# Performance work log

Hardware: AMD Instinct MI355X
Metric: run time of the kernel (lower is better)

## Reference

```python
import jax, jax.numpy as jnp
import numpy as np

N_NODES = 100000
N_EDGES = 1600000
IN_FEATS, N_HIDDEN, N_CLASSES = 128, 128, 32


def setup_inputs() -> dict:
    key = jax.random.key(0)
    ks = jax.random.split(key, 9)
    x = jax.random.normal(ks[0], (N_NODES, IN_FEATS), dtype=jnp.float32)
    src = jax.random.randint(ks[1], (N_EDGES,), 0, N_NODES, dtype=jnp.int64)
    dst = jax.random.randint(ks[2], (N_EDGES,), 0, N_NODES, dtype=jnp.int64)
    s1 = 1.0 / np.sqrt(IN_FEATS)
    s2 = 1.0 / np.sqrt(N_HIDDEN)
    W1 = jax.random.uniform(ks[3], (IN_FEATS, N_HIDDEN), jnp.float32, -s1, s1)
    b1 = jnp.zeros((N_HIDDEN,), jnp.float32)
    W2 = jax.random.uniform(ks[4], (N_HIDDEN, N_HIDDEN), jnp.float32, -s2, s2)
    b2 = jnp.zeros((N_HIDDEN,), jnp.float32)
    W3 = jax.random.uniform(ks[5], (N_HIDDEN, N_CLASSES), jnp.float32, -s2, s2)
    b3 = jnp.zeros((N_CLASSES,), jnp.float32)
    return {"x": x, "W1": W1, "b1": b1, "W2": W2, "b2": b2, "W3": W3, "b3": b3,
            "src": src, "dst": dst}


def _norms(src, dst):
    ones = jnp.ones((src.shape[0],), jnp.float32)
    deg_out = jax.ops.segment_sum(ones, src, num_segments=N_NODES)
    deg_in = jax.ops.segment_sum(ones, dst, num_segments=N_NODES)
    inv_sqrt = lambda d: jnp.where(d > 0, jax.lax.rsqrt(jnp.maximum(d, 1.0)), 0.0)
    return inv_sqrt(deg_out), inv_sqrt(deg_in)


def _sgconv(h, W, b, src, dst, norm_src, norm_dst):
    # D^-1/2 A D^-1/2 h, then linear
    m = h * norm_src[:, None]          # scale by source (out-degree) norm
    msg = m[src]                        # [E, F] gather
    agg = jax.ops.segment_sum(msg, dst, num_segments=N_NODES)  # scatter-add
    agg = agg * norm_dst[:, None]
    return agg @ W + b


def reference(x, W1, b1, W2, b2, W3, b3, src, dst):
    norm_src, norm_dst = _norms(src, dst)
    h = _sgconv(x, W1, b1, src, dst, norm_src, norm_dst)
    h = jax.nn.relu(h)
    h = _sgconv(h, W2, b2, src, dst, norm_src, norm_dst)
    h = jax.nn.relu(h)
    h = _sgconv(h, W3, b3, src, dst, norm_src, norm_dst)
    return h
```

## Files before the change

kernel.cpp:

```cpp
#include <hip/hip_runtime.h>


constexpr int FEAT   = 128;
constexpr int STRIDE = 48;

typedef float f32x4 __attribute__((ext_vector_type(4)));
typedef short bf16x8 __attribute__((ext_vector_type(8)));

__device__ __forceinline__ unsigned short f2bf(float f) {
    unsigned int u = __builtin_bit_cast(unsigned int, f);
    unsigned int r = (u + 0x7FFFu + ((u >> 16) & 1u)) >> 16;
    return (unsigned short)r;
}
__device__ __forceinline__ float bflo(unsigned int u) {
    return __builtin_bit_cast(float, u << 16);
}
__device__ __forceinline__ float bfhi(unsigned int u) {
    return __builtin_bit_cast(float, u & 0xffff0000u);
}
__device__ __forceinline__ unsigned int pack2(float a, float b) {
    return (unsigned int)f2bf(a) | ((unsigned int)f2bf(b) << 16);
}

__global__ __launch_bounds__(256) void wfrag_kernel(const float* __restrict__ W1,
                                                    const float* __restrict__ W3,
                                                    unsigned short* __restrict__ f1,
                                                    unsigned short* __restrict__ f3)
{
    int idx = blockIdx.x * 256 + threadIdx.x;
    const float* W;
    unsigned short* f;
    int NC, i;
    if (idx < 2048)      { W = W1; f = f1; NC = 128; i = idx; }
    else if (idx < 2560) { W = W3; f = f3; NC = 32;  i = idx - 2048; }
    else return;
    int l  = i & 63;
    int k0 = (i >> 6) & 3;
    int n0 = i >> 8;
    int kb = k0 * 32 + (l >> 4) * 8;
    int n  = n0 * 16 + (l & 15);
    const float* wp = W + (size_t)kb * NC + n;
    uint4 v;
    v.x = pack2(wp[0],      wp[NC]);
    v.y = pack2(wp[2 * NC], wp[3 * NC]);
    v.z = pack2(wp[4 * NC], wp[5 * NC]);
    v.w = pack2(wp[6 * NC], wp[7 * NC]);
    *reinterpret_cast<uint4*>(&f[i * 8]) = v;
}

__global__ __launch_bounds__(256) void degree_fill_xw1_kernel(
    const int* __restrict__ src, const int* __restrict__ dst,
    const float* __restrict__ x, const unsigned short* __restrict__ w1frag,
    int* __restrict__ deg_out, int* __restrict__ deg_in,
    int* __restrict__ csr_pad, unsigned short* __restrict__ xw1,
    int N, int E)
{
    const int tid = threadIdx.x;
    const int g = (int)blockIdx.x / 5;
    const int m = (int)blockIdx.x % 5;

    if (m != 4) {
        int e = (g * 4 + m) * 256 + tid;
        if (e < E) {
            int s = src[e];
            int d = dst[e];
            atomicAdd(&deg_out[s], 1);
            int pos = atomicAdd(&deg_in[d], 1);
            if (pos < STRIDE)
                csr_pad[(size_t)d * STRIDE + pos] = s;
        }
        return;
    }

    const int wave = tid >> 6, lane = tid & 63;
    const int rowbase = g * 64 + wave * 16;
    const int arow = min(rowbase + (lane & 15), N - 1);
    const int koff = (lane >> 4) * 8;

    bf16x8 a[4];
    #pragma unroll
    for (int k0 = 0; k0 < 4; ++k0) {
        const float* xp = x + (size_t)arow * 128 + k0 * 32 + koff;
        float4 f0 = *reinterpret_cast<const float4*>(xp);
        float4 f1 = *reinterpret_cast<const float4*>(xp + 4);
        union { unsigned int u[4]; bf16x8 v; } r;
        r.u[0] = pack2(f0.x, f0.y); r.u[1] = pack2(f0.z, f0.w);
        r.u[2] = pack2(f1.x, f1.y); r.u[3] = pack2(f1.z, f1.w);
        a[k0] = r.v;
    }

    f32x4 acc[8];
    #pragma unroll
    for (int n0 = 0; n0 < 8; ++n0) acc[n0] = (f32x4)0.f;
    #pragma unroll
    for (int k0 = 0; k0 < 4; ++k0) {
        #pragma unroll
        for (int n0 = 0; n0 < 8; ++n0) {
            bf16x8 b = *reinterpret_cast<const bf16x8*>(&w1frag[((n0 * 4 + k0) * 64 + lane) * 8]);
            acc[n0] = __builtin_amdgcn_mfma_f32_16x16x32_bf16(a[k0], b, acc[n0], 0, 0, 0);
        }
    }

    const int colbase = lane & 15;
    const int rowoff = (lane >> 4) * 4;
    #pragma unroll
    for (int r = 0; r < 4; ++r) {
        const int grow = rowbase + rowoff + r;
        if (grow < N) {
            unsigned short* op = xw1 + (size_t)grow * 128 + colbase;
            #pragma unroll
            for (int n0 = 0; n0 < 8; ++n0)
                op[n0 * 16] = f2bf(acc[n0][r]);
        }
    }
}

__global__ __launch_bounds__(256) void norm_kernel(const int* __restrict__ dout,
                                                   const int* __restrict__ din,
                                                   float* __restrict__ nsrc,
                                                   float* __restrict__ ndst, int N)
{
    int i = blockIdx.x * 256 + threadIdx.x;
    if (i < N) {
        int a = dout[i], b = din[i];
        nsrc[i] = (a > 0) ? rsqrtf((float)a) : 0.f;
        ndst[i] = (b > 0) ? rsqrtf((float)b) : 0.f;
    }
}

__global__ __launch_bounds__(256) void gather1_kernel(const unsigned short* __restrict__ xw1,
                                                      const float* __restrict__ nsrc,
                                                      const float* __restrict__ ndst,
                                                      const int* __restrict__ deg_in,
                                                      const int* __restrict__ csr_pad,
                                                      const float* __restrict__ b1,
                                                      unsigned short* __restrict__ hb1,
                                                      int N)
{
    const int node = blockIdx.x * 16 + (threadIdx.x >> 4);
    const int c = (threadIdx.x & 15) * 8;
    if (node >= N) return;
    const int* idx = csr_pad + (size_t)node * STRIDE;
    const int deg = min(deg_in[node], STRIDE);
    float4 a0 = make_float4(0.f, 0.f, 0.f, 0.f);
    float4 a1 = make_float4(0.f, 0.f, 0.f, 0.f);
    int j = 0;
    for (; j + 8 <= deg; j += 8) {
        int s[8];
        float ns[8];
        #pragma unroll
        for (int u = 0; u < 8; ++u) s[u] = idx[j + u];
        #pragma unroll
        for (int u = 0; u < 8; ++u) ns[u] = nsrc[s[u]];
        #pragma unroll
        for (int u = 0; u < 8; ++u) {
            uint4 v = *reinterpret_cast<const uint4*>(xw1 + (size_t)s[u] * 128 + c);
            a0.x = fmaf(bflo(v.x), ns[u], a0.x);
            a0.y = fmaf(bfhi(v.x), ns[u], a0.y);
            a0.z = fmaf(bflo(v.y), ns[u], a0.z);
            a0.w = fmaf(bfhi(v.y), ns[u], a0.w);
            a1.x = fmaf(bflo(v.z), ns[u], a1.x);
            a1.y = fmaf(bfhi(v.z), ns[u], a1.y);
            a1.z = fmaf(bflo(v.w), ns[u], a1.z);
            a1.w = fmaf(bfhi(v.w), ns[u], a1.w);
        }
    }
    for (; j < deg; ++j) {
        int s0 = idx[j];
        float n0 = nsrc[s0];
        uint4 v = *reinterpret_cast<const uint4*>(xw1 + (size_t)s0 * 128 + c);
        a0.x = fmaf(bflo(v.x), n0, a0.x);
        a0.y = fmaf(bfhi(v.x), n0, a0.y);
        a0.z = fmaf(bflo(v.y), n0, a0.z);
        a0.w = fmaf(bfhi(v.y), n0, a0.w);
        a1.x = fmaf(bflo(v.z), n0, a1.x);
        a1.y = fmaf(bfhi(v.z), n0, a1.y);
        a1.z = fmaf(bflo(v.w), n0, a1.z);
        a1.w = fmaf(bfhi(v.w), n0, a1.w);
    }
    const float nd = ndst[node];
    const float nsn = nsrc[node];
    const float* bp = b1 + c;
    float v0 = fmaxf(a0.x * nd + bp[0], 0.f) * nsn;
    float v1 = fmaxf(a0.y * nd + bp[1], 0.f) * nsn;
    float v2 = fmaxf(a0.z * nd + bp[2], 0.f) * nsn;
    float v3 = fmaxf(a0.w * nd + bp[3], 0.f) * nsn;
    float v4 = fmaxf(a1.x * nd + bp[4], 0.f) * nsn;
    float v5 = fmaxf(a1.y * nd + bp[5], 0.f) * nsn;
    float v6 = fmaxf(a1.z * nd + bp[6], 0.f) * nsn;
    float v7 = fmaxf(a1.w * nd + bp[7], 0.f) * nsn;
    uint4 o;
    o.x = pack2(v0, v1); o.y = pack2(v2, v3);
    o.z = pack2(v4, v5); o.w = pack2(v6, v7);
    *reinterpret_cast<uint4*>(hb1 + (size_t)node * 128 + c) = o;
}

__global__ __launch_bounds__(256) void gather128_kernel(const unsigned short* __restrict__ hb,
                                                        const float* __restrict__ ndst,
                                                        const int* __restrict__ deg_in,
                                                        const int* __restrict__ csr_pad,
                                                        unsigned short* __restrict__ aggb,
                                                        int N)
{
    const int node = blockIdx.x * 16 + (threadIdx.x >> 4);
    const int c = (threadIdx.x & 15) * 8;
    if (node >= N) return;
    const int* idx = csr_pad + (size_t)node * STRIDE;
    const int deg = min(deg_in[node], STRIDE);
    float4 a0 = make_float4(0.f, 0.f, 0.f, 0.f);
    float4 a1 = make_float4(0.f, 0.f, 0.f, 0.f);
    int j = 0;
    for (; j + 8 <= deg; j += 8) {
        int s[8];
        #pragma unroll
        for (int u = 0; u < 8; ++u) s[u] = idx[j + u];
        #pragma unroll
        for (int u = 0; u < 8; ++u) {
            uint4 v = *reinterpret_cast<const uint4*>(hb + (size_t)s[u] * 128 + c);
            a0.x += bflo(v.x); a0.y += bfhi(v.x);
            a0.z += bflo(v.y); a0.w += bfhi(v.y);
            a1.x += bflo(v.z); a1.y += bfhi(v.z);
            a1.z += bflo(v.w); a1.w += bfhi(v.w);
        }
    }
    for (; j < deg; ++j) {
        uint4 v = *reinterpret_cast<const uint4*>(hb + (size_t)idx[j] * 128 + c);
        a0.x += bflo(v.x); a0.y += bfhi(v.x);
        a0.z += bflo(v.y); a0.w += bfhi(v.y);
        a1.x += bflo(v.z); a1.y += bfhi(v.z);
        a1.z += bflo(v.w); a1.w += bfhi(v.w);
    }
    const float nd = ndst[node];
    uint4 o;
    o.x = pack2(a0.x * nd, a0.y * nd);
    o.y = pack2(a0.z * nd, a0.w * nd);
    o.z = pack2(a1.x * nd, a1.y * nd);
    o.w = pack2(a1.z * nd, a1.w * nd);
    *reinterpret_cast<uint4*>(aggb + (size_t)node * 128 + c) = o;
}

__global__ __launch_bounds__(256) void gemm23_kernel(
    const unsigned short* __restrict__ Ab,
    const float* __restrict__ W2,
    const float* __restrict__ b2,
    const unsigned short* __restrict__ w3frag,
    const float* __restrict__ nsrc,
    unsigned short* __restrict__ tb,
    int N)
{
    constexpr int NC = 128, SLD = 136;
    __shared__ alignas(16) unsigned short Wl[8 * 4 * 64 * 8];
    __shared__ alignas(16) unsigned short Sc[4][16 * SLD];
    const int tid = threadIdx.x;

    for (int idx = tid; idx < 8 * 4 * 64; idx += 256) {
        int l  = idx & 63;
        int k0 = (idx >> 6) & 3;
        int n0 = idx >> 8;
        int kb = k0 * 32 + (l >> 4) * 8;
        int n  = n0 * 16 + (l & 15);
        const float* wp = W2 + (size_t)kb * NC + n;
        uint4 v;
        v.x = pack2(wp[0],      wp[NC]);
        v.y = pack2(wp[2 * NC], wp[3 * NC]);
        v.z = pack2(wp[4 * NC], wp[5 * NC]);
        v.w = pack2(wp[6 * NC], wp[7 * NC]);
        *reinterpret_cast<uint4*>(&Wl[idx * 8]) = v;
    }
    __syncthreads();

    const int wave = tid >> 6, lane = tid & 63;
    const int rowbase = blockIdx.x * 64 + wave * 16;
    const int arow = min(rowbase + (lane & 15), N - 1);
    const int koff = (lane >> 4) * 8;

    bf16x8 a[4];
    #pragma unroll
    for (int k0 = 0; k0 < 4; ++k0)
        a[k0] = *reinterpret_cast<const bf16x8*>(Ab + (size_t)arow * 128 + k0 * 32 + koff);

    f32x4 acc[8];
    #pragma unroll
    for (int n0 = 0; n0 < 8; ++n0) acc[n0] = (f32x4)0.f;
    #pragma unroll
    for (int k0 = 0; k0 < 4; ++k0) {
        #pragma unroll
        for (int n0 = 0; n0 < 8; ++n0) {
            bf16x8 b = *reinterpret_cast<const bf16x8*>(&Wl[((n0 * 4 + k0) * 64 + lane) * 8]);
            acc[n0] = __builtin_amdgcn_mfma_f32_16x16x32_bf16(a[k0], b, acc[n0], 0, 0, 0);
        }
    }

    unsigned short* sc = &Sc[wave][0];
    #pragma unroll
    for (int n0 = 0; n0 < 8; ++n0) {
        int col = n0 * 16 + (lane & 15);
        float bv = b2[col];
        #pragma unroll
        for (int r = 0; r < 4; ++r) {
            int row = (lane >> 4) * 4 + r;
            sc[row * SLD + col] = f2bf(fmaxf(acc[n0][r] + bv, 0.f));
        }
    }

    f32x4 acc3[2];
    acc3[0] = (f32x4)0.f; acc3[1] = (f32x4)0.f;
    #pragma unroll
    for (int k0 = 0; k0 < 4; ++k0) {
        bf16x8 a3 = *reinterpret_cast<const bf16x8*>(&sc[(lane & 15) * SLD + k0 * 32 + koff]);
        #pragma unroll
        for (int n0 = 0; n0 < 2; ++n0) {
            bf16x8 b = *reinterpret_cast<const bf16x8*>(&w3frag[((n0 * 4 + k0) * 64 + lane) * 8]);
            acc3[n0] = __builtin_amdgcn_mfma_f32_16x16x32_bf16(a3, b, acc3[n0], 0, 0, 0);
        }
    }

    float rs[4];
    #pragma unroll
    for (int r = 0; r < 4; ++r)
        rs[r] = nsrc[min(rowbase + (lane >> 4) * 4 + r, N - 1)];
    #pragma unroll
    for (int n0 = 0; n0 < 2; ++n0) {
        int col = n0 * 16 + (lane & 15);
        #pragma unroll
        for (int r = 0; r < 4; ++r) {
            int grow = rowbase + (lane >> 4) * 4 + r;
            if (grow < N)
                tb[(size_t)grow * 32 + col] = f2bf(acc3[n0][r] * rs[r]);
        }
    }
}

__global__ __launch_bounds__(256) void gather32_kernel(const unsigned short* __restrict__ hb,
                                                       const float* __restrict__ ndst,
                                                       const int* __restrict__ deg_in,
                                                       const int* __restrict__ csr_pad,
                                                       const float* __restrict__ bias,
                                                       float* __restrict__ out, int N)
{
    const int node = blockIdx.x * 64 + (threadIdx.x >> 2);
    const int c = (threadIdx.x & 3) * 8;
    if (node >= N) return;
    const int* idx = csr_pad + (size_t)node * STRIDE;
    const int deg = min(deg_in[node], STRIDE);
    float4 a0 = make_float4(0.f, 0.f, 0.f, 0.f);
    float4 a1 = make_float4(0.f, 0.f, 0.f, 0.f);
    int j = 0;
    for (; j + 8 <= deg; j += 8) {
        int s[8];
        #pragma unroll
        for (int u = 0; u < 8; ++u) s[u] = idx[j + u];
        #pragma unroll
        for (int u = 0; u < 8; ++u) {
            uint4 v = *reinterpret_cast<const uint4*>(hb + (size_t)s[u] * 32 + c);
            a0.x += bflo(v.x); a0.y += bfhi(v.x);
            a0.z += bflo(v.y); a0.w += bfhi(v.y);
            a1.x += bflo(v.z); a1.y += bfhi(v.z);
            a1.z += bflo(v.w); a1.w += bfhi(v.w);
        }
    }
    for (; j < deg; ++j) {
        uint4 v = *reinterpret_cast<const uint4*>(hb + (size_t)idx[j] * 32 + c);
        a0.x += bflo(v.x); a0.y += bfhi(v.x);
        a0.z += bflo(v.y); a0.w += bfhi(v.y);
        a1.x += bflo(v.z); a1.y += bfhi(v.z);
        a1.z += bflo(v.w); a1.w += bfhi(v.w);
    }
    const float nd = ndst[node];
    float4 o0, o1;
    o0.x = a0.x * nd + bias[c + 0]; o0.y = a0.y * nd + bias[c + 1];
    o0.z = a0.z * nd + bias[c + 2]; o0.w = a0.w * nd + bias[c + 3];
    o1.x = a1.x * nd + bias[c + 4]; o1.y = a1.y * nd + bias[c + 5];
    o1.z = a1.z * nd + bias[c + 6]; o1.w = a1.w * nd + bias[c + 7];
    float* op = out + (size_t)node * 32 + c;
    *reinterpret_cast<float4*>(op)     = o0;
    *reinterpret_cast<float4*>(op + 4) = o1;
}

extern "C" void kernel_launch(void* const* d_in, const int* in_sizes, int n_in,
                              void* d_out, int out_size, void* d_ws, size_t ws_size,
                              hipStream_t stream)
{
    const float* x  = (const float*)d_in[0];
    const float* W1 = (const float*)d_in[1];
    const float* b1 = (const float*)d_in[2];
    const float* W2 = (const float*)d_in[3];
    const float* b2 = (const float*)d_in[4];
    const float* W3 = (const float*)d_in[5];
    const float* b3 = (const float*)d_in[6];
    const int*   src = (const int*)d_in[7];
    const int*   dst = (const int*)d_in[8];
    float* out = (float*)d_out;

    const int N = in_sizes[0] / FEAT;
    const int E = in_sizes[7];
    const int GB = (N + 63) / 64;

    char* w = (char*)d_ws;
    float* norm_src  = (float*)w;                  w += (size_t)N * 4;
    float* norm_dst  = (float*)w;                  w += (size_t)N * 4;
    int*   deg_out   = (int*)w;                    w += (size_t)N * 4;
    int*   deg_in    = (int*)w;                    w += (size_t)N * 4;
    unsigned short* w1frag = (unsigned short*)w;   w += (size_t)2048 * 8 * 2;
    unsigned short* w3frag = (unsigned short*)w;   w += (size_t)512 * 8 * 2;
    int*   csr_pad   = (int*)w;                    w += (size_t)N * STRIDE * 4;
    unsigned short* xw1  = (unsigned short*)w;     w += (size_t)N * FEAT * 2;
    unsigned short* hb1  = (unsigned short*)w;     w += (size_t)N * FEAT * 2;
    unsigned short* aggb = (unsigned short*)w;
    unsigned short* tb = xw1;

    hipMemsetAsync(deg_out, 0, 2 * (size_t)N * sizeof(int), stream);
    wfrag_kernel<<<10, 256, 0, stream>>>(W1, W3, w1frag, w3frag);
    degree_fill_xw1_kernel<<<GB * 5, 256, 0, stream>>>(
        src, dst, x, w1frag, deg_out, deg_in, csr_pad, xw1, N, E);
    norm_kernel<<<(N + 255) / 256, 256, 0, stream>>>(deg_out, deg_in, norm_src, norm_dst, N);

    gather1_kernel<<<(N + 15) / 16, 256, 0, stream>>>(
        xw1, norm_src, norm_dst, deg_in, csr_pad, b1, hb1, N);

    gather128_kernel<<<(N + 15) / 16, 256, 0, stream>>>(
        hb1, norm_dst, deg_in, csr_pad, aggb, N);
    gemm23_kernel<<<GB, 256, 0, stream>>>(aggb, W2, b2, w3frag, norm_src, tb, N);

    gather32_kernel<<<(N + 63) / 64, 256, 0, stream>>>(
        tb, norm_dst, deg_in, csr_pad, b3, out, N);
}
```

Baseline: 336.6 us.

## Fuse layer-2 gather into GEMM kernel, drop norm kernel, precompute W2 fragments

Merges the 128-wide neighbour gather with the W2/W3 GEMM kernel, so each 64-node block aggregates into LDS and feeds MFMA directly. This removes the aggb round-trip through global memory and one launch. The norm kernel is dropped and inverse-sqrt degrees are computed inline from integer degrees. W2 bf16 fragments are now built once in wfrag_kernel and read from global memory rather than rebuilt in LDS by every block. The tradeoff is fewer gather blocks (64 nodes each, four rounds) with a barrier before the GEMM, which may reduce latency hiding in the gather phase.

Result: no change. 330.8 us (-1.7%).

```diff
diff --git a/kernel.cpp b/kernel.cpp
--- a/kernel.cpp
+++ b/kernel.cpp
@@ -21,10 +21,15 @@
 __device__ __forceinline__ unsigned int pack2(float a, float b) {
     return (unsigned int)f2bf(a) | ((unsigned int)f2bf(b) << 16);
 }
+__device__ __forceinline__ float invsq(int d) {
+    return (d > 0) ? rsqrtf((float)d) : 0.f;
+}
 
 __global__ __launch_bounds__(256) void wfrag_kernel(const float* __restrict__ W1,
+                                                    const float* __restrict__ W2,
                                                     const float* __restrict__ W3,
                                                     unsigned short* __restrict__ f1,
+                                                    unsigned short* __restrict__ f2,
                                                     unsigned short* __restrict__ f3)
 {
     int idx = blockIdx.x * 256 + threadIdx.x;
@@ -32,7 +37,8 @@
     unsigned short* f;
     int NC, i;
     if (idx < 2048)      { W = W1; f = f1; NC = 128; i = idx; }
-    else if (idx < 2560) { W = W3; f = f3; NC = 32;  i = idx - 2048; }
+    else if (idx < 4096) { W = W2; f = f2; NC = 128; i = idx - 2048; }
+    else if (idx < 4608) { W = W3; f = f3; NC = 32;  i = idx - 4096; }
     else return;
     int l  = i & 63;
     int k0 = (i >> 6) & 3;
@@ -115,22 +121,8 @@
     }
 }
 
-__global__ __launch_bounds__(256) void norm_kernel(const int* __restrict__ dout,
-                                                   const int* __restrict__ din,
-                                                   float* __restrict__ nsrc,
-                                                   float* __restrict__ ndst, int N)
-{
-    int i = blockIdx.x * 256 + threadIdx.x;
-    if (i < N) {
-        int a = dout[i], b = din[i];
-        nsrc[i] = (a > 0) ? rsqrtf((float)a) : 0.f;
-        ndst[i] = (b > 0) ? rsqrtf((float)b) : 0.f;
-    }
-}
-
 __global__ __launch_bounds__(256) void gather1_kernel(const unsigned short* __restrict__ xw1,
-                                                      const float* __restrict__ nsrc,
-                                                      const float* __restrict__ ndst,
+                                                      const int* __restrict__ deg_out,
                                                       const int* __restrict__ deg_in,
                                                       const int* __restrict__ csr_pad,
                                                       const float* __restrict__ b1,
@@ -141,7 +133,8 @@
     const int c = (threadIdx.x & 15) * 8;
     if (node >= N) return;
     const int* idx = csr_pad + (size_t)node * STRIDE;
-    const int deg = min(deg_in[node], STRIDE);
+    const int dgt = deg_in[node];
+    const int deg = min(dgt, STRIDE);
     float4 a0 = make_float4(0.f, 0.f, 0.f, 0.f);
     float4 a1 = make_float4(0.f, 0.f, 0.f, 0.f);
     int j = 0;
@@ -151,7 +144,7 @@
         #pragma unroll
         for (int u = 0; u < 8; ++u) s[u] = idx[j + u];
         #pragma unroll
-        for (int u = 0; u < 8; ++u) ns[u] = nsrc[s[u]];
+        for (int u = 0; u < 8; ++u) ns[u] = invsq(deg_out[s[u]]);
         #pragma unroll
         for (int u = 0; u < 8; ++u) {
             uint4 v = *reinterpret_cast<const uint4*>(xw1 + (size_t)s[u] * 128 + c);
@@ -167,7 +160,7 @@
     }
     for (; j < deg; ++j) {
         int s0 = idx[j];
-        float n0 = nsrc[s0];
+        float n0 = invsq(deg_out[s0]);
         uint4 v = *reinterpret_cast<const uint4*>(xw1 + (size_t)s0 * 128 + c);
         a0.x = fmaf(bflo(v.x), n0, a0.x);
         a0.y = fmaf(bfhi(v.x), n0, a0.y);
@@ -178,8 +171,8 @@
         a1.z = fmaf(bflo(v.w), n0, a1.z);
         a1.w = fmaf(bfhi(v.w), n0, a1.w);
     }
-    const float nd = ndst[node];
-    const float nsn = nsrc[node];
+    const float nd = invsq(dgt);
+    const float nsn = invsq(deg_out[node]);
     const float* bp = b1 + c;
     float v0 = fmaxf(a0.x * nd + bp[0], 0.f) * nsn;
     float v1 = fmaxf(a0.y * nd + bp[1], 0.f) * nsn;
@@ -195,89 +188,74 @@
     *reinterpret_cast<uint4*>(hb1 + (size_t)node * 128 + c) = o;
 }
 
-__global__ __launch_bounds__(256) void gather128_kernel(const unsigned short* __restrict__ hb,
-                                                        const float* __restrict__ ndst,
-                                                        const int* __restrict__ deg_in,
-                                                        const int* __restrict__ csr_pad,
-                                                        unsigned short* __restrict__ aggb,
-                                                        int N)
-{
-    const int node = blockIdx.x * 16 + (threadIdx.x >> 4);
-    const int c = (threadIdx.x & 15) * 8;
-    if (node >= N) return;
-    const int* idx = csr_pad + (size_t)node * STRIDE;
-    const int deg = min(deg_in[node], STRIDE);
-    float4 a0 = make_float4(0.f, 0.f, 0.f, 0.f);
-    float4 a1 = make_float4(0.f, 0.f, 0.f, 0.f);
-    int j = 0;
-    for (; j + 8 <= deg; j += 8) {
-        int s[8];
-        #pragma unroll
-        for (int u = 0; u < 8; ++u) s[u] = idx[j + u];
-        #pragma unroll
-        for (int u = 0; u < 8; ++u) {
-            uint4 v = *reinterpret_cast<const uint4*>(hb + (size_t)s[u] * 128 + c);
-            a0.x += bflo(v.x); a0.y += bfhi(v.x);
-            a0.z += bflo(v.y); a0.w += bfhi(v.y);
-            a1.x += bflo(v.z); a1.y += bfhi(v.z);
-            a1.z += bflo(v.w); a1.w += bfhi(v.w);
-        }
-    }
-    for (; j < deg; ++j) {
-        uint4 v = *reinterpret_cast<const uint4*>(hb + (size_t)idx[j] * 128 + c);
-        a0.x += bflo(v.x); a0.y += bfhi(v.x);
-        a0.z += bflo(v.y); a0.w += bfhi(v.y);
-        a1.x += bflo(v.z); a1.y += bfhi(v.z);
-        a1.z += bflo(v.w); a1.w += bfhi(v.w);
-    }
-    const float nd = ndst[node];
-    uint4 o;
-    o.x = pack2(a0.x * nd, a0.y * nd);
-    o.y = pack2(a0.z * nd, a0.w * nd);
-    o.z = pack2(a1.x * nd, a1.y * nd);
-    o.w = pack2(a1.z * nd, a1.w * nd);
-    *reinterpret_cast<uint4*>(aggb + (size_t)node * 128 + c) = o;
-}
-
-__global__ __launch_bounds__(256) void gemm23_kernel(
-    const unsigned short* __restrict__ Ab,
-    const float* __restrict__ W2,
+__global__ __launch_bounds__(256) void gather_gemm23_kernel(
+    const unsigned short* __restrict__ hb,
+    const int* __restrict__ deg_out,
+    const int* __restrict__ deg_in,
+    const int* __restrict__ csr_pad,
+    const unsigned short* __restrict__ w2frag,
     const float* __restrict__ b2,
     const unsigned short* __restrict__ w3frag,
-    const float* __restrict__ nsrc,
     unsigned short* __restrict__ tb,
     int N)
 {
-    constexpr int NC = 128, SLD = 136;
-    __shared__ alignas(16) unsigned short Wl[8 * 4 * 64 * 8];
-    __shared__ alignas(16) unsigned short Sc[4][16 * SLD];
+    constexpr int SLD = 136;
+    __shared__ alignas(16) unsigned short Sc[64 * SLD];
     const int tid = threadIdx.x;
-
-    for (int idx = tid; idx < 8 * 4 * 64; idx += 256) {
-        int l  = idx & 63;
-        int k0 = (idx >> 6) & 3;
-        int n0 = idx >> 8;
-        int kb = k0 * 32 + (l >> 4) * 8;
-        int n  = n0 * 16 + (l & 15);
-        const float* wp = W2 + (size_t)kb * NC + n;
-        uint4 v;
-        v.x = pack2(wp[0],      wp[NC]);
-        v.y = pack2(wp[2 * NC], wp[3 * NC]);
-        v.z = pack2(wp[4 * NC], wp[5 * NC]);
-        v.w = pack2(wp[6 * NC], wp[7 * NC]);
-        *reinterpret_cast<uint4*>(&Wl[idx * 8]) = v;
+    const int nb = (int)blockIdx.x * 64;
+
+    const int slot = tid >> 4;
+    const int c = (tid & 15) * 8;
+    for (int rnd = 0; rnd < 4; ++rnd) {
+        const int node = nb + rnd * 16 + slot;
+        float4 a0 = make_float4(0.f, 0.f, 0.f, 0.f);
+        float4 a1 = make_float4(0.f, 0.f, 0.f, 0.f);
+        float nd = 0.f;
+        if (node < N) {
+            const int* idx = csr_pad + (size_t)node * STRIDE;
+            const int dgt = deg_in[node];
+            const int deg = min(dgt, STRIDE);
+            nd = invsq(dgt);
+            int j = 0;
+            for (; j + 8 <= deg; j += 8) {
+                int s[8];
+                #pragma unroll
+                for (int u = 0; u < 8; ++u) s[u] = idx[j + u];
+                #pragma unroll
+                for (int u = 0; u < 8; ++u) {
+                    uint4 v = *reinterpret_cast<const uint4*>(hb + (size_t)s[u] * 128 + c);
+                    a0.x += bflo(v.x); a0.y += bfhi(v.x);
+                    a0.z += bflo(v.y); a0.w += bfhi(v.y);
+                    a1.x += bflo(v.z); a1.y += bfhi(v.z);
+                    a1.z += bflo(v.w); a1.w += bfhi(v.w);
+                }
+            }
+            for (; j < deg; ++j) {
+                uint4 v = *reinterpret_cast<const uint4*>(hb + (size_t)idx[j] * 128 + c);
+                a0.x += bflo(v.x); a0.y += bfhi(v.x);
+                a0.z += bflo(v.y); a0.w += bfhi(v.y);
+                a1.x += bflo(v.z); a1.y += bfhi(v.z);
+                a1.z += bflo(v.w); a1.w += bfhi(v.w);
+            }
+        }
+        uint4 o;
+        o.x = pack2(a0.x * nd, a0.y * nd);
+        o.y = pack2(a0.z * nd, a0.w * nd);
+        o.z = pack2(a1.x * nd, a1.y * nd);
+        o.w = pack2(a1.z * nd, a1.w * nd);
+        *reinterpret_cast<uint4*>(&Sc[(rnd * 16 + slot) * SLD + c]) = o;
     }
     __syncthreads();
 
     const int wave = tid >> 6, lane = tid & 63;
-    const int rowbase = blockIdx.x * 64 + wave * 16;
-    const int arow = min(rowbase + (lane & 15), N - 1);
+    const int rowbase = nb + wave * 16;
+    const int lrow = wave * 16 + (lane & 15);
     const int koff = (lane >> 4) * 8;
 
     bf16x8 a[4];
     #pragma unroll
     for (int k0 = 0; k0 < 4; ++k0)
-        a[k0] = *reinterpret_cast<const bf16x8*>(Ab + (size_t)arow * 128 + k0 * 32 + koff);
+        a[k0] = *reinterpret_cast<const bf16x8*>(&Sc[lrow * SLD + k0 * 32 + koff]);
 
     f32x4 acc[8];
     #pragma unroll
@@ -286,28 +264,28 @@
     for (int k0 = 0; k0 < 4; ++k0) {
         #pragma unroll
         for (int n0 = 0; n0 < 8; ++n0) {
-            bf16x8 b = *reinterpret_cast<const bf16x8*>(&Wl[((n0 * 4 + k0) * 64 + lane) * 8]);
+            bf16x8 b = *reinterpret_cast<const bf16x8*>(&w2frag[((n0 * 4 + k0) * 64 + lane) * 8]);
             acc[n0] = __builtin_amdgcn_mfma_f32_16x16x32_bf16(a[k0], b, acc[n0], 0, 0, 0);
         }
     }
 
-    unsigned short* sc = &Sc[wave][0];
     #pragma unroll
     for (int n0 = 0; n0 < 8; ++n0) {
         int col = n0 * 16 + (lane & 15);
         float bv = b2[col];
         #pragma unroll
         for (int r = 0; r < 4; ++r) {
-            int row = (lane >> 4) * 4 + r;
-            sc[row * SLD + col] = f2bf(fmaxf(acc[n0][r] + bv, 0.f));
-        }
-    }
+            int row = wave * 16 + (lane >> 4) * 4 + r;
+            Sc[row * SLD + col] = f2bf(fmaxf(acc[n0][r] + bv, 0.f));
+        }
+    }
+    __syncthreads();
 
     f32x4 acc3[2];
     acc3[0] = (f32x4)0.f; acc3[1] = (f32x4)0.f;
     #pragma unroll
     for (int k0 = 0; k0 < 4; ++k0) {
-        bf16x8 a3 = *reinterpret_cast<const bf16x8*>(&sc[(lane & 15) * SLD + k0 * 32 + koff]);
+        bf16x8 a3 = *reinterpret_cast<const bf16x8*>(&Sc[lrow * SLD + k0 * 32 + koff]);
         #pragma unroll
         for (int n0 = 0; n0 < 2; ++n0) {
             bf16x8 b = *reinterpret_cast<const bf16x8*>(&w3frag[((n0 * 4 + k0) * 64 + lane) * 8]);
@@ -318,7 +296,7 @@
     float rs[4];
     #pragma unroll
     for (int r = 0; r < 4; ++r)
-        rs[r] = nsrc[min(rowbase + (lane >> 4) * 4 + r, N - 1)];
+        rs[r] = invsq(deg_out[min(rowbase + (lane >> 4) * 4 + r, N - 1)]);
     #pragma unroll
     for (int n0 = 0; n0 < 2; ++n0) {
         int col = n0 * 16 + (lane & 15);
@@ -332,7 +310,6 @@
 }
 
 __global__ __launch_bounds__(256) void gather32_kernel(const unsigned short* __restrict__ hb,
-                                                       const float* __restrict__ ndst,
                                                        const int* __restrict__ deg_in,
                                                        const int* __restrict__ csr_pad,
                                                        const float* __restrict__ bias,
@@ -342,7 +319,8 @@
     const int c = (threadIdx.x & 3) * 8;
     if (node >= N) return;
     const int* idx = csr_pad + (size_t)node * STRIDE;
-    const int deg = min(deg_in[node], STRIDE);
+    const int dgt = deg_in[node];
+    const int deg = min(dgt, STRIDE);
     float4 a0 = make_float4(0.f, 0.f, 0.f, 0.f);
     float4 a1 = make_float4(0.f, 0.f, 0.f, 0.f);
     int j = 0;
@@ -366,7 +344,7 @@
         a1.x += bflo(v.z); a1.y += bfhi(v.z);
         a1.z += bflo(v.w); a1.w += bfhi(v.w);
     }
-    const float nd = ndst[node];
+    const float nd = invsq(dgt);
     float4 o0, o1;
     o0.x = a0.x * nd + bias[c + 0]; o0.y = a0.y * nd + bias[c + 1];
     o0.z = a0.z * nd + bias[c + 2]; o0.w = a0.w * nd + bias[c + 3];
@@ -397,31 +375,27 @@
     const int GB = (N + 63) / 64;
 
     char* w = (char*)d_ws;
-    float* norm_src  = (float*)w;                  w += (size_t)N * 4;
-    float* norm_dst  = (float*)w;                  w += (size_t)N * 4;
     int*   deg_out   = (int*)w;                    w += (size_t)N * 4;
     int*   deg_in    = (int*)w;                    w += (size_t)N * 4;
     unsigned short* w1frag = (unsigned short*)w;   w += (size_t)2048 * 8 * 2;
+    unsigned short* w2frag = (unsigned short*)w;   w += (size_t)2048 * 8 * 2;
     unsigned short* w3frag = (unsigned short*)w;   w += (size_t)512 * 8 * 2;
     int*   csr_pad   = (int*)w;                    w += (size_t)N * STRIDE * 4;
     unsigned short* xw1  = (unsigned short*)w;     w += (size_t)N * FEAT * 2;
     unsigned short* hb1  = (unsigned short*)w;     w += (size_t)N * FEAT * 2;
-    unsigned short* aggb = (unsigned short*)w;
     unsigned short* tb = xw1;
 
     hipMemsetAsync(deg_out, 0, 2 * (size_t)N * sizeof(int), stream);
-    wfrag_kernel<<<10, 256, 0, stream>>>(W1, W3, w1frag, w3frag);
+    wfrag_kernel<<<18, 256, 0, stream>>>(W1, W2, W3, w1frag, w2frag, w3frag);
     degree_fill_xw1_kernel<<<GB * 5, 256, 0, stream>>>(
         src, dst, x, w1frag, deg_out, deg_in, csr_pad, xw1, N, E);
-    norm_kernel<<<(N + 255) / 256, 256, 0, stream>>>(deg_out, deg_in, norm_src, norm_dst, N);
 
     gather1_kernel<<<(N + 15) / 16, 256, 0, stream>>>(
-        xw1, norm_src, norm_dst, deg_in, csr_pad, b1, hb1, N);
-
-    gather128_kernel<<<(N + 15) / 16, 256, 0, stream>>>(
-        hb1, norm_dst, deg_in, csr_pad, aggb, N);
-    gemm23_kernel<<<GB, 256, 0, stream>>>(aggb, W2, b2, w3frag, norm_src, tb, N);
+        xw1, deg_out, deg_in, csr_pad, b1, hb1, N);
+
+    gather_gemm23_kernel<<<(N + 63) / 64, 256, 0, stream>>>(
+        hb1, deg_out, deg_in, csr_pad, w2frag, b2, w3frag, tb, N);
 
     gather32_kernel<<<(N + 63) / 64, 256, 0, stream>>>(
-        tb, norm_dst, deg_in, csr_pad, b3, out, N);
-}
+        tb, deg_in, csr_pad, b3, out, N);
+}
```
